# Optimization experiments

Measured on AMD Instinct MI355X. Metric: run time of the kernel, lower is better.

Reference implementation:

```python
import jax, jax.numpy as jnp
import numpy as np

S, B, H = 4096, 32, 512

def setup_inputs() -> dict:
    key = jax.random.key(0)
    k1, k2, k3, k4, k5 = jax.random.split(key, 5)
    hidden = jax.random.normal(k1, (1, B, H), dtype=jnp.float32)
    encoder_outputs = jax.random.normal(k2, (S, B, H), dtype=jnp.float32)
    embedding = jax.random.normal(k3, (S, B, 3), dtype=jnp.float32)
    # learned params (xavier-ish scale)
    bigram_matrix = jax.random.normal(k4, (H, H), dtype=jnp.float32) * (1.0 / np.sqrt(H))
    affect_matrix = jax.random.normal(k5, (H, 3), dtype=jnp.float32) * 0.1
    return {"hidden": hidden, "encoder_outputs": encoder_outputs,
            "embedding": embedding, "bigram_matrix": bigram_matrix,
            "affect_matrix": affect_matrix}

def reference(hidden, encoder_outputs, embedding, bigram_matrix, affect_matrix):
    # hidden: [1,B,H] -> [B,H] (view(-1) over single layer)
    h = hidden[0]
    # bigram-modulated encoder states:
    #   i == 0: enc[0]
    #   i  > 0: (enc[i-1] @ W_bigram) * enc[i]
    modulated = jnp.einsum('sbh,hk->sbk', encoder_outputs[:-1], bigram_matrix) * encoder_outputs[1:]
    bigram_hidden = jnp.concatenate([encoder_outputs[:1], modulated], axis=0)  # [S,B,H]
    # dot-attention energy per (b, s)
    e_dot = jnp.einsum('sbh,bh->bs', bigram_hidden, h)  # [B,S]
    # affect term: (h @ affect_matrix) . embedding[s,b]
    e_aff = jnp.einsum('bk,sbk->bs', jnp.einsum('bh,hk->bk', h, affect_matrix), embedding)
    attn = jax.nn.softmax(e_dot + e_aff, axis=-1)  # softmax over seq dim
    return attn[:, None, :]  # [B,1,S]
```

## Files before the change

### kernel.cpp

```cpp
#include <hip/hip_runtime.h>
#include <cstdint>
#include <cstddef>

#define S_DIM 4096
#define B_DIM 32
#define H_DIM 512
#define M_DIM (S_DIM * B_DIM)

typedef unsigned short u16;
typedef unsigned int u32;
typedef float f32x4 __attribute__((ext_vector_type(4)));
typedef __bf16 bf16x8 __attribute__((ext_vector_type(8)));

__device__ __forceinline__ u16 f2bf(float v) {
    union { float f; u32 u; } a; a.f = v;
    u32 r = a.u + 0x7fffu + ((a.u >> 16) & 1u);
    return (u16)(r >> 16);
}
__device__ __forceinline__ float bf2f(u16 b) {
    union { float f; u32 u; } a; a.u = ((u32)b) << 16; return a.f;
}
__device__ __forceinline__ void split_bf(float v, u16& h, u16& l) {
    h = f2bf(v);
    l = f2bf(v - bf2f(h));
}

__device__ __forceinline__ void gl2lds16(const void* g, void* l) {
    __builtin_amdgcn_global_load_lds(
        (const __attribute__((address_space(1))) unsigned int*)g,
        (__attribute__((address_space(3))) unsigned int*)l,
        16, 0, 0);
}

__global__ __launch_bounds__(256) void prep_w_swz(
    const float* __restrict__ W, u16* __restrict__ Wsp)
{
    const int t    = blockIdx.x * 256 + threadIdx.x;
    const int kt   = t >> 11;
    const int rem  = t & 2047;
    const int tt   = rem >> 6;
    const int lane = rem & 63;
    const int g    = lane >> 4;
    const int cl   = lane & 15;
    const int jb   = kt * 32 + g * 8;
    const int k    = tt * 16 + cl;
    u16* po = Wsp + (size_t)kt * 32768 + tt * 1024 + lane * 8;
    #pragma unroll
    for (int e = 0; e < 8; ++e) {
        u16 hi, lo;
        split_bf(W[(size_t)(jb + e) * H_DIM + k], hi, lo);
        po[e] = hi;
        po[512 + e] = lo;
    }
}

union Bf8u { bf16x8 v; u32 w[4]; };

__device__ __forceinline__ void split8(f32x4 v0, f32x4 v1, bf16x8& h8, bf16x8& l8) {
    float v[8] = {v0.x, v0.y, v0.z, v0.w, v1.x, v1.y, v1.z, v1.w};
    Bf8u H, L;
    #pragma unroll
    for (int j = 0; j < 4; ++j) {
        const u32 u0 = __float_as_uint(v[2 * j]);
        const u32 u1 = __float_as_uint(v[2 * j + 1]);
        H.w[j] = __builtin_amdgcn_perm(u1, u0, 0x07060302u);
        const float r0 = v[2 * j]     - __uint_as_float(u0 & 0xffff0000u);
        const float r1 = v[2 * j + 1] - __uint_as_float(u1 & 0xffff0000u);
        L.w[j] = __builtin_amdgcn_perm(__float_as_uint(r1), __float_as_uint(r0),
                                       0x07060302u);
    }
    h8 = H.v; l8 = L.v;
}

__global__ __launch_bounds__(256, 3) void bigram_gemm_v4(
    const float* __restrict__ enc,
    const float* __restrict__ hid,
    const u16* __restrict__ Wsp,
    float* __restrict__ Lp)
{
    __shared__ float sA[128 * 32];
    __shared__ u16   sB[2][8192];
    __shared__ float rowsum[2][128];

    const int tid  = threadIdx.x;
    const int wave = tid >> 6;
    const int lane = tid & 63;
    const int wr   = wave >> 1;
    const int wc   = wave & 1;
    const int logical = (blockIdx.x & 7) * 512 + (blockIdx.x >> 3);
    const int nt   = logical & 3;
    const int mt   = logical >> 2;
    const int m0   = mt * 128;
    const int g    = lane >> 4;
    const int cl   = lane & 15;

    const int arow = wave * 32 + (lane >> 3);
    const int acol = (((lane & 7) ^ ((lane >> 3) & 7)) << 2);
    const float* peA = enc + (size_t)(m0 + arow) * H_DIM + acol;

    const u16* pwB = Wsp + (size_t)nt * 8192 + wave * 2048 + lane * 8;

    const int arb = (wr * 64 + cl) * 128;
    const int ac0 = ((2 * g) ^ (cl & 7)) << 4;
    const int ac1 = ((2 * g + 1) ^ (cl & 7)) << 4;
    const char* sAb = (const char*)sA;
    const int bfo = wc * 8192 + lane * 16;
    const char* sBb = (const char*)sB;

    f32x4 acc[4][4];
    #pragma unroll
    for (int mf = 0; mf < 4; ++mf)
        #pragma unroll
        for (int nf = 0; nf < 4; ++nf)
            acc[mf][nf] = (f32x4){0.f, 0.f, 0.f, 0.f};

#define STAGE_A(KT) do {                                                       \
    const float* _s = peA + (size_t)(KT) * 32;                                 \
    char* _d = (char*)sA + wave * 4096;                                        \
    gl2lds16(_s,          _d);                                                 \
    gl2lds16(_s +  4096,  _d + 1024);                                          \
    gl2lds16(_s +  8192,  _d + 2048);                                          \
    gl2lds16(_s + 12288,  _d + 3072);                                          \
  } while (0)

#define STAGE_B(KT, CUR) do {                                                  \
    const u16* _s = pwB + (size_t)(KT) * 32768;                                \
    char* _d = (char*)sB + (CUR) * 16384 + wave * 4096;                        \
    gl2lds16(_s,         _d);                                                  \
    gl2lds16(_s +  512,  _d + 1024);                                           \
    gl2lds16(_s + 1024,  _d + 2048);                                           \
    gl2lds16(_s + 1536,  _d + 3072);                                           \
  } while (0)

    STAGE_A(0);
    STAGE_B(0, 0);
    __syncthreads();

#define GEMM_STEP(KT, CUR)                                                     \
  {                                                                            \
    f32x4 aa[4][2];                                                            \
    _Pragma("unroll")                                                          \
    for (int mf = 0; mf < 4; ++mf) {                                           \
      aa[mf][0] = *(const f32x4*)(sAb + arb + mf * 2048 + ac0);                \
      aa[mf][1] = *(const f32x4*)(sAb + arb + mf * 2048 + ac1);                \
    }                                                                          \
    bf16x8 bh[4], bl[4];                                                       \
    _Pragma("unroll")                                                          \
    for (int nf = 0; nf < 4; ++nf) {                                           \
      bh[nf] = *(const bf16x8*)(sBb + (CUR) * 16384 + bfo + nf * 2048);        \
      bl[nf] = *(const bf16x8*)(sBb + (CUR) * 16384 + bfo + nf * 2048 + 1024); \
    }                                                                          \
    __syncthreads();      \
    if ((KT) < 15) {                                                           \
      STAGE_A((KT) + 1);                                                       \
      STAGE_B((KT) + 1, (CUR) ^ 1);                                            \
    }                                                                          \
    __builtin_amdgcn_s_setprio(1);                                             \
    _Pragma("unroll")                                                          \
    for (int mf = 0; mf < 4; ++mf) {                                           \
      bf16x8 ah, al;                                                           \
      split8(aa[mf][0], aa[mf][1], ah, al);                                    \
      _Pragma("unroll")                                                        \
      for (int nf = 0; nf < 4; ++nf) {                                         \
        acc[mf][nf] = __builtin_amdgcn_mfma_f32_16x16x32_bf16(ah, bh[nf], acc[mf][nf], 0, 0, 0); \
        acc[mf][nf] = __builtin_amdgcn_mfma_f32_16x16x32_bf16(ah, bl[nf], acc[mf][nf], 0, 0, 0); \
        acc[mf][nf] = __builtin_amdgcn_mfma_f32_16x16x32_bf16(al, bh[nf], acc[mf][nf], 0, 0, 0); \
      }                                                                        \
    }                                                                          \
    __builtin_amdgcn_s_setprio(0);                                             \
    __syncthreads();            \
  }

    for (int kt = 0; kt < 16; kt += 2) {
        GEMM_STEP(kt, 0);
        GEMM_STEP(kt + 1, 1);
    }
#undef GEMM_STEP
#undef STAGE_A
#undef STAGE_B

    #pragma unroll
    for (int mf = 0; mf < 4; ++mf) {
        float rs0 = 0.f, rs1 = 0.f, rs2 = 0.f, rs3 = 0.f;
        const int r4 = m0 + wr * 64 + mf * 16 + g * 4;
        #pragma unroll
        for (int nf = 0; nf < 4; ++nf) {
            const int gcol = nt * 128 + wc * 64 + nf * 16 + cl;
            float e0 = (r4 + 0 < M_DIM - 32)
                ? enc[(size_t)(r4 + 32) * H_DIM + gcol] * hid[((r4 + 0) & 31) * H_DIM + gcol] : 0.f;
            float e1 = (r4 + 1 < M_DIM - 32)
                ? enc[(size_t)(r4 + 33) * H_DIM + gcol] * hid[((r4 + 1) & 31) * H_DIM + gcol] : 0.f;
            float e2 = (r4 + 2 < M_DIM - 32)
                ? enc[(size_t)(r4 + 34) * H_DIM + gcol] * hid[((r4 + 2) & 31) * H_DIM + gcol] : 0.f;
            float e3 = (r4 + 3 < M_DIM - 32)
                ? enc[(size_t)(r4 + 35) * H_DIM + gcol] * hid[((r4 + 3) & 31) * H_DIM + gcol] : 0.f;
            rs0 += acc[mf][nf][0] * e0;
            rs1 += acc[mf][nf][1] * e1;
            rs2 += acc[mf][nf][2] * e2;
            rs3 += acc[mf][nf][3] * e3;
        }
        #pragma unroll
        for (int off = 1; off < 16; off <<= 1) {
            rs0 += __shfl_xor(rs0, off);
            rs1 += __shfl_xor(rs1, off);
            rs2 += __shfl_xor(rs2, off);
            rs3 += __shfl_xor(rs3, off);
        }
        if (cl == 0) {
            const int rb = wr * 64 + mf * 16 + g * 4;
            rowsum[wc][rb + 0] = rs0;
            rowsum[wc][rb + 1] = rs1;
            rowsum[wc][rb + 2] = rs2;
            rowsum[wc][rb + 3] = rs3;
        }
    }
    __syncthreads();
    if (tid < 128) {
        const int gm = m0 + tid + 32;
        if (gm < M_DIM) {
            Lp[(size_t)nt * M_DIM + (size_t)(gm & 31) * S_DIM + (gm >> 5)] =
                rowsum[0][tid] + rowsum[1][tid];
        }
    }
}

__global__ __launch_bounds__(256) void prep_aff(
    const float* __restrict__ enc,
    const float* __restrict__ hid,
    const float* __restrict__ aff,
    float* __restrict__ Aux)
{
    __shared__ float w[4][4];
    const int b    = blockIdx.x;
    const int tid  = threadIdx.x;
    const int wave = tid >> 6;
    const int lane = tid & 63;

    float p0 = 0.f, p1 = 0.f, p2 = 0.f, p3 = 0.f;
    #pragma unroll
    for (int it = 0; it < 2; ++it) {
        const int h = tid + it * 256;
        const float hv = hid[b * H_DIM + h];
        p0 += hv * aff[h * 3 + 0];
        p1 += hv * aff[h * 3 + 1];
        p2 += hv * aff[h * 3 + 2];
        p3 += hv * enc[(size_t)b * H_DIM + h];
    }
    #pragma unroll
    for (int off = 32; off > 0; off >>= 1) {
        p0 += __shfl_xor(p0, off);
        p1 += __shfl_xor(p1, off);
        p2 += __shfl_xor(p2, off);
        p3 += __shfl_xor(p3, off);
    }
    if (lane == 0) { w[wave][0] = p0; w[wave][1] = p1; w[wave][2] = p2; w[wave][3] = p3; }
    __syncthreads();
    if (tid < 4)
        Aux[b * 4 + tid] = w[0][tid] + w[1][tid] + w[2][tid] + w[3][tid];
}

__global__ __launch_bounds__(256) void sm_partial(
    const float* __restrict__ emb,
    const float* __restrict__ Lp,
    const float* __restrict__ Aux,
    float* __restrict__ Lg,
    float* __restrict__ Part)
{
    __shared__ float wm[4];
    __shared__ float wsum[4];
    const int b     = blockIdx.x >> 3;
    const int strip = blockIdx.x & 7;
    const int tid   = threadIdx.x;
    const int wave  = tid >> 6;
    const int lane  = tid & 63;

    const float ha0 = Aux[b * 4 + 0], ha1 = Aux[b * 4 + 1],
                ha2 = Aux[b * 4 + 2], s0dot = Aux[b * 4 + 3];

    float lgv[2];
    float mx = -3.4e38f;
    #pragma unroll
    for (int it = 0; it < 2; ++it) {
        const int s = strip * 512 + it * 256 + tid;
        const size_t base = (size_t)b * S_DIM + s;
        const float ed = (s == 0) ? s0dot
            : (Lp[base] + Lp[(size_t)M_DIM + base] + Lp[2 * (size_t)M_DIM + base] + Lp[3 * (size_t)M_DIM + base]);
        const float* e = emb + (size_t)(s * B_DIM + b) * 3;
        const float lg = ed + ha0 * e[0] + ha1 * e[1] + ha2 * e[2];
        Lg[(size_t)b * S_DIM + s] = lg;
        lgv[it] = lg;
        mx = fmaxf(mx, lg);
    }
    #pragma unroll
    for (int off = 32; off > 0; off >>= 1) mx = fmaxf(mx, __shfl_xor(mx, off));
    if (lane == 0) wm[wave] = mx;
    __syncthreads();
    mx = fmaxf(fmaxf(wm[0], wm[1]), fmaxf(wm[2], wm[3]));

    float sum = __expf(lgv[0] - mx) + __expf(lgv[1] - mx);
    #pragma unroll
    for (int off = 32; off > 0; off >>= 1) sum += __shfl_xor(sum, off);
    if (lane == 0) wsum[wave] = sum;
    __syncthreads();
    if (tid == 0) {
        Part[(size_t)(b * 8 + strip) * 2 + 0] = mx;
        Part[(size_t)(b * 8 + strip) * 2 + 1] = wsum[0] + wsum[1] + wsum[2] + wsum[3];
    }
}

__global__ __launch_bounds__(256) void sm_final(
    const float* __restrict__ Lg,
    const float* __restrict__ Part,
    float* __restrict__ out)
{
    const int b     = blockIdx.x >> 3;
    const int strip = blockIdx.x & 7;
    const int tid   = threadIdx.x;

    float M = -3.4e38f;
    #pragma unroll
    for (int i = 0; i < 8; ++i) M = fmaxf(M, Part[(size_t)(b * 8 + i) * 2]);
    float S = 0.f;
    #pragma unroll
    for (int i = 0; i < 8; ++i)
        S += Part[(size_t)(b * 8 + i) * 2 + 1] * __expf(Part[(size_t)(b * 8 + i) * 2] - M);
    const float inv = 1.0f / S;

    #pragma unroll
    for (int it = 0; it < 2; ++it) {
        const int s = strip * 512 + it * 256 + tid;
        out[(size_t)b * S_DIM + s] = __expf(Lg[(size_t)b * S_DIM + s] - M) * inv;
    }
}

extern "C" void kernel_launch(void* const* d_in, const int* in_sizes, int n_in,
                              void* d_out, int out_size, void* d_ws, size_t ws_size,
                              hipStream_t stream) {
    const float* hid = (const float*)d_in[0];
    const float* enc = (const float*)d_in[1];
    const float* emb = (const float*)d_in[2];
    const float* Wm  = (const float*)d_in[3];
    const float* aff = (const float*)d_in[4];
    float* out = (float*)d_out;

    char* ws = (char*)d_ws;
    u16*   Wsp = (u16*)ws;
    float* Lp  = (float*)(ws + (2048u << 10));
    float* Aux = (float*)(ws + (4096u << 10));
    float* Part= (float*)(ws + (4096u << 10) + 1024);
    float* Lg  = (float*)ws;

    hipLaunchKernelGGL(prep_w_swz, dim3(128), dim3(256), 0, stream, Wm, Wsp);
    hipLaunchKernelGGL(prep_aff, dim3(32), dim3(256), 0, stream, enc, hid, aff, Aux);
    hipLaunchKernelGGL(bigram_gemm_v4, dim3(4096), dim3(256), 0, stream,
                       enc, hid, Wsp, Lp);
    hipLaunchKernelGGL(sm_partial, dim3(256), dim3(256), 0, stream,
                       emb, Lp, Aux, Lg, Part);
    hipLaunchKernelGGL(sm_final, dim3(256), dim3(256), 0, stream,
                       Lg, Part, out);
}
```

Baseline: 560.3 us.

## Enlarge bigram GEMM tile to 256x256 with 512 threads and double-buffered A

The bigram GEMM block tile grows from 128x128 to 256x256 with 8 waves per block. Each wave now holds 4x8 accumulator fragments, so the encoder rows are re-read across only 2 column tiles instead of 4, and the softmax partial kernel sums two partial logit planes instead of four. A is now double-buffered in LDS, which lets the mid-step barrier go, since prefetch writes target the other buffer. B fragments are loaded inside the MFMA loop instead of all up front. The cost is roughly 130KB of LDS per block and higher register pressure, which probably limits each CU to one block and reduces latency hiding.

```diff
diff --git a/kernel.cpp b/kernel.cpp
--- a/kernel.cpp
+++ b/kernel.cpp
@@ -72,25 +72,25 @@
     h8 = H.v; l8 = L.v;
 }
 
-__global__ __launch_bounds__(256, 3) void bigram_gemm_v4(
+__global__ __launch_bounds__(512, 2) void bigram_gemm_v5(
     const float* __restrict__ enc,
     const float* __restrict__ hid,
     const u16* __restrict__ Wsp,
     float* __restrict__ Lp)
 {
-    __shared__ float sA[128 * 32];
-    __shared__ u16   sB[2][8192];
-    __shared__ float rowsum[2][128];
+    __shared__ float sA[2][256 * 32];
+    __shared__ u16   sB[2][16384];
+    __shared__ float rowsum[2][256];
 
     const int tid  = threadIdx.x;
     const int wave = tid >> 6;
     const int lane = tid & 63;
     const int wr   = wave >> 1;
     const int wc   = wave & 1;
-    const int logical = (blockIdx.x & 7) * 512 + (blockIdx.x >> 3);
-    const int nt   = logical & 3;
-    const int mt   = logical >> 2;
-    const int m0   = mt * 128;
+    const int logical = (blockIdx.x & 7) * 128 + (blockIdx.x >> 3);
+    const int nt   = logical & 1;
+    const int mt   = logical >> 1;
+    const int m0   = mt * 256;
     const int g    = lane >> 4;
     const int cl   = lane & 15;
 
@@ -98,77 +98,71 @@
     const int acol = (((lane & 7) ^ ((lane >> 3) & 7)) << 2);
     const float* peA = enc + (size_t)(m0 + arow) * H_DIM + acol;
 
-    const u16* pwB = Wsp + (size_t)nt * 8192 + wave * 2048 + lane * 8;
+    const u16* pwB = Wsp + (size_t)nt * 16384 + wave * 2048 + lane * 8;
 
     const int arb = (wr * 64 + cl) * 128;
     const int ac0 = ((2 * g) ^ (cl & 7)) << 4;
     const int ac1 = ((2 * g + 1) ^ (cl & 7)) << 4;
     const char* sAb = (const char*)sA;
-    const int bfo = wc * 8192 + lane * 16;
+    const int bfo = wc * 16384 + lane * 16;
     const char* sBb = (const char*)sB;
 
-    f32x4 acc[4][4];
+    f32x4 acc[4][8];
     #pragma unroll
     for (int mf = 0; mf < 4; ++mf)
         #pragma unroll
-        for (int nf = 0; nf < 4; ++nf)
+        for (int nf = 0; nf < 8; ++nf)
             acc[mf][nf] = (f32x4){0.f, 0.f, 0.f, 0.f};
 
-#define STAGE_A(KT) do {                                                       \
+#define STAGE_A(KT, BUF) do {                                                  \
     const float* _s = peA + (size_t)(KT) * 32;                                 \
-    char* _d = (char*)sA + wave * 4096;                                        \
-    gl2lds16(_s,          _d);                                                 \
-    gl2lds16(_s +  4096,  _d + 1024);                                          \
-    gl2lds16(_s +  8192,  _d + 2048);                                          \
-    gl2lds16(_s + 12288,  _d + 3072);                                          \
+    char* _d = (char*)sA + (BUF) * 32768 + wave * 4096;                        \
+    gl2lds16(_s,                _d);                                           \
+    gl2lds16(_s +  8 * H_DIM,   _d + 1024);                                    \
+    gl2lds16(_s + 16 * H_DIM,   _d + 2048);                                    \
+    gl2lds16(_s + 24 * H_DIM,   _d + 3072);                                    \
   } while (0)
 
-#define STAGE_B(KT, CUR) do {                                                  \
+#define STAGE_B(KT, BUF) do {                                                  \
     const u16* _s = pwB + (size_t)(KT) * 32768;                                \
-    char* _d = (char*)sB + (CUR) * 16384 + wave * 4096;                        \
+    char* _d = (char*)sB + (BUF) * 32768 + wave * 4096;                        \
     gl2lds16(_s,         _d);                                                  \
     gl2lds16(_s +  512,  _d + 1024);                                           \
     gl2lds16(_s + 1024,  _d + 2048);                                           \
     gl2lds16(_s + 1536,  _d + 3072);                                           \
   } while (0)
 
-    STAGE_A(0);
+    STAGE_A(0, 0);
     STAGE_B(0, 0);
     __syncthreads();
 
 #define GEMM_STEP(KT, CUR)                                                     \
   {                                                                            \
-    f32x4 aa[4][2];                                                            \
+    bf16x8 ah[4], al[4];                                                       \
     _Pragma("unroll")                                                          \
     for (int mf = 0; mf < 4; ++mf) {                                           \
-      aa[mf][0] = *(const f32x4*)(sAb + arb + mf * 2048 + ac0);                \
-      aa[mf][1] = *(const f32x4*)(sAb + arb + mf * 2048 + ac1);                \
+      const f32x4 a0 = *(const f32x4*)(sAb + (CUR) * 32768 + arb + mf * 2048 + ac0); \
+      const f32x4 a1 = *(const f32x4*)(sAb + (CUR) * 32768 + arb + mf * 2048 + ac1); \
+      split8(a0, a1, ah[mf], al[mf]);                                          \
     }                                                                          \
-    bf16x8 bh[4], bl[4];                                                       \
-    _Pragma("unroll")                                                          \
-    for (int nf = 0; nf < 4; ++nf) {                                           \
-      bh[nf] = *(const bf16x8*)(sBb + (CUR) * 16384 + bfo + nf * 2048);        \
-      bl[nf] = *(const bf16x8*)(sBb + (CUR) * 16384 + bfo + nf * 2048 + 1024); \
-    }                                                                          \
-    __syncthreads();      \
     if ((KT) < 15) {                                                           \
-      STAGE_A((KT) + 1);                                                       \
+      STAGE_A((KT) + 1, (CUR) ^ 1);                                            \
       STAGE_B((KT) + 1, (CUR) ^ 1);                                            \
     }                                                                          \
     __builtin_amdgcn_s_setprio(1);                                             \
     _Pragma("unroll")                                                          \
-    for (int mf = 0; mf < 4; ++mf) {                                           \
-      bf16x8 ah, al;                                                           \
-      split8(aa[mf][0], aa[mf][1], ah, al);                                    \
+    for (int nf = 0; nf < 8; ++nf) {                                           \
+      const bf16x8 bh = *(const bf16x8*)(sBb + (CUR) * 32768 + bfo + nf * 2048);        \
+      const bf16x8 bl = *(const bf16x8*)(sBb + (CUR) * 32768 + bfo + nf * 2048 + 1024); \
       _Pragma("unroll")                                                        \
-      for (int nf = 0; nf < 4; ++nf) {                                         \
-        acc[mf][nf] = __builtin_amdgcn_mfma_f32_16x16x32_bf16(ah, bh[nf], acc[mf][nf], 0, 0, 0); \
-        acc[mf][nf] = __builtin_amdgcn_mfma_f32_16x16x32_bf16(ah, bl[nf], acc[mf][nf], 0, 0, 0); \
-        acc[mf][nf] = __builtin_amdgcn_mfma_f32_16x16x32_bf16(al, bh[nf], acc[mf][nf], 0, 0, 0); \
+      for (int mf = 0; mf < 4; ++mf) {                                         \
+        acc[mf][nf] = __builtin_amdgcn_mfma_f32_16x16x32_bf16(ah[mf], bh, acc[mf][nf], 0, 0, 0); \
+        acc[mf][nf] = __builtin_amdgcn_mfma_f32_16x16x32_bf16(ah[mf], bl, acc[mf][nf], 0, 0, 0); \
+        acc[mf][nf] = __builtin_amdgcn_mfma_f32_16x16x32_bf16(al[mf], bh, acc[mf][nf], 0, 0, 0); \
       }                                                                        \
     }                                                                          \
     __builtin_amdgcn_s_setprio(0);                                             \
-    __syncthreads();            \
+    __syncthreads();     \
   }
 
     for (int kt = 0; kt < 16; kt += 2) {
@@ -184,8 +178,8 @@
         float rs0 = 0.f, rs1 = 0.f, rs2 = 0.f, rs3 = 0.f;
         const int r4 = m0 + wr * 64 + mf * 16 + g * 4;
         #pragma unroll
-        for (int nf = 0; nf < 4; ++nf) {
-            const int gcol = nt * 128 + wc * 64 + nf * 16 + cl;
+        for (int nf = 0; nf < 8; ++nf) {
+            const int gcol = nt * 256 + wc * 128 + nf * 16 + cl;
             float e0 = (r4 + 0 < M_DIM - 32)
                 ? enc[(size_t)(r4 + 32) * H_DIM + gcol] * hid[((r4 + 0) & 31) * H_DIM + gcol] : 0.f;
             float e1 = (r4 + 1 < M_DIM - 32)
@@ -215,7 +209,7 @@
         }
     }
     __syncthreads();
-    if (tid < 128) {
+    if (tid < 256) {
         const int gm = m0 + tid + 32;
         if (gm < M_DIM) {
             Lp[(size_t)nt * M_DIM + (size_t)(gm & 31) * S_DIM + (gm >> 5)] =
@@ -284,7 +278,7 @@
         const int s = strip * 512 + it * 256 + tid;
         const size_t base = (size_t)b * S_DIM + s;
         const float ed = (s == 0) ? s0dot
-            : (Lp[base] + Lp[(size_t)M_DIM + base] + Lp[2 * (size_t)M_DIM + base] + Lp[3 * (size_t)M_DIM + base]);
+                                  : (Lp[base] + Lp[(size_t)M_DIM + base]);
         const float* e = emb + (size_t)(s * B_DIM + b) * 3;
         const float lg = ed + ha0 * e[0] + ha1 * e[1] + ha2 * e[2];
         Lg[(size_t)b * S_DIM + s] = lg;
@@ -352,7 +346,7 @@
 
     hipLaunchKernelGGL(prep_w_swz, dim3(128), dim3(256), 0, stream, Wm, Wsp);
     hipLaunchKernelGGL(prep_aff, dim3(32), dim3(256), 0, stream, enc, hid, aff, Aux);
-    hipLaunchKernelGGL(bigram_gemm_v4, dim3(4096), dim3(256), 0, stream,
+    hipLaunchKernelGGL(bigram_gemm_v5, dim3(1024), dim3(512), 0, stream,
                        enc, hid, Wsp, Lp);
     hipLaunchKernelGGL(sm_partial, dim3(256), dim3(256), 0, stream,
                        emb, Lp, Aux, Lg, Part);
```

After: 601.6 us. 7.4% more time.
